# Optimization experiments

Hardware: AMD Instinct MI355X
Metric: run time of the kernel (lower is better)

The kernel has to match this reference:

```python
import jax, jax.numpy as jnp
import numpy as np

M_CENTER = 3.0  # diagonal value of the 'centers' matrix
OUT_HW = (513, 513)  # original input spatial size (input_shape in torch forward)


def _conv(x, w, dilation=1, padding=0):
    return jax.lax.conv_general_dilated(
        x, w, window_strides=(1, 1),
        padding=[(padding, padding), (padding, padding)],
        rhs_dilation=(dilation, dilation),
        dimension_numbers=("NCHW", "OIHW", "NCHW"))


def _resize(x, hw):
    return jax.image.resize(x, (x.shape[0], x.shape[1], hw[0], hw[1]), method="bilinear")


def _head(low_level, out, pw, w0, w1, w2, w3, pool_w, aproj_w, cw1, cw2, cb2):
    # DeepLabHeadV3Plus (BN folded to identity at inference: gamma=1, beta=0, mean=0, var=1)
    ll = jax.nn.relu(_conv(low_level, pw))                      # [N,48,129,129]
    branches = [jax.nn.relu(_conv(out, w0))]                    # 1x1 branch
    for w, d in zip((w1, w2, w3), (6, 12, 18)):
        branches.append(jax.nn.relu(_conv(out, w, dilation=d, padding=d)))
    gp = jnp.mean(out, axis=(2, 3), keepdims=True)              # AdaptiveAvgPool2d(1)
    gp = jax.nn.relu(_conv(gp, pool_w))
    gp = jnp.broadcast_to(gp, branches[0].shape)                # bilinear upsample of 1x1 == broadcast
    branches.append(gp)
    y = jax.nn.relu(_conv(jnp.concatenate(branches, axis=1), aproj_w))  # [N,256,33,33]
    y = _resize(y, (ll.shape[2], ll.shape[3]))                  # -> 129x129
    y = jnp.concatenate([ll, y], axis=1)                        # [N,304,129,129]
    y = jax.nn.relu(_conv(y, cw1, padding=1))
    y = _conv(y, cw2) + cb2[None, :, None, None]                # [N,C,129,129]
    return y


def _forward_single(x):
    # x: [N,C,129,129] head logits. Upsample, then squared-distance to diagonal centers (m*I).
    x = _resize(x, OUT_HW)                                      # [N,C,513,513]
    C = x.shape[1]
    features_out = jnp.transpose(x, (0, 2, 3, 1))               # NHWC, as in torch
    # dist2mean[...,c] = -sum_j (f_j - m*1[j==c])^2 = -(|f|^2 - 2*m*f_c + m^2)
    sumsq = jnp.sum(x * x, axis=1, keepdims=True)
    logits = 2.0 * M_CENTER * x - sumsq - M_CENTER * M_CENTER   # [N,C,513,513]
    centers = M_CENTER * jnp.eye(C, dtype=x.dtype)
    return logits, centers, features_out


def _kaiming(key, shape):
    fan_in = shape[1] * shape[2] * shape[3]
    return jax.random.normal(key, shape, jnp.float32) * np.sqrt(2.0 / fan_in)


def _head_params(key, num_classes):
    ks = jax.random.split(key, 10)
    return dict(
        pw=_kaiming(ks[0], (48, 256, 1, 1)),
        w0=_kaiming(ks[1], (256, 2048, 1, 1)),
        w1=_kaiming(ks[2], (256, 2048, 3, 3)),
        w2=_kaiming(ks[3], (256, 2048, 3, 3)),
        w3=_kaiming(ks[4], (256, 2048, 3, 3)),
        pool_w=_kaiming(ks[5], (256, 2048, 1, 1)),
        aproj_w=_kaiming(ks[6], (256, 1280, 1, 1)),
        cw1=_kaiming(ks[7], (256, 304, 3, 3)),
        cw2=_kaiming(ks[8], (num_classes, 256, 1, 1)),
        cb2=jnp.zeros((num_classes,), jnp.float32),
    )


def setup_inputs() -> dict:
    key = jax.random.key(0)
    k_ll, k_out, k_h0, k_h1 = jax.random.split(key, 4)
    inp = {
        "low_level": jax.random.normal(k_ll, (2, 256, 129, 129), jnp.float32),
        "out": jax.random.normal(k_out, (2, 2048, 33, 33), jnp.float32),
    }
    for pref, k, nc in (("h0_", k_h0, 16), ("h1_", k_h1, 17)):
        for name, v in _head_params(k, nc).items():
            inp[pref + name] = v
    return inp


def reference(low_level, out,
              h0_pw, h0_w0, h0_w1, h0_w2, h0_w3, h0_pool_w, h0_aproj_w, h0_cw1, h0_cw2, h0_cb2,
              h1_pw, h1_w0, h1_w1, h1_w2, h1_w3, h1_pool_w, h1_aproj_w, h1_cw1, h1_cw2, h1_cb2):
    x0 = _head(low_level, out, h0_pw, h0_w0, h0_w1, h0_w2, h0_w3, h0_pool_w, h0_aproj_w, h0_cw1, h0_cw2, h0_cb2)
    x1 = _head(low_level, out, h1_pw, h1_w0, h1_w1, h1_w2, h1_w3, h1_pool_w, h1_aproj_w, h1_cw1, h1_cw2, h1_cb2)
    l0, c0, f0 = _forward_single(x0)
    l1, c1, f1 = _forward_single(x1)
    return (l0, l1, c0, c1, f0, f1)
```

## Files before the change

### kernel.cpp

```cpp
#include <hip/hip_runtime.h>

#define TPB 256

typedef _Float16 f16;
typedef __attribute__((ext_vector_type(8))) _Float16 f16x8;
typedef __attribute__((ext_vector_type(16))) float f32x16;

#define GLD_LDS(g, l) __builtin_amdgcn_global_load_lds( \
    (const __attribute__((address_space(1))) void*)(g), \
    (__attribute__((address_space(3))) void*)(l), 16, 0, 0)

__global__ __launch_bounds__(TPB)
void tcz_k(const float* __restrict__ aspp, const float* __restrict__ ll,
           f16* __restrict__ Xa, f16* __restrict__ Xll, float* __restrict__ gp)
{
    const int bid = blockIdx.x;
    const int tid = threadIdx.x;
    __shared__ float t32[32 * 33];
    __shared__ float red[4];
    if (bid >= 12816) {
        const int bc = bid - 12816;
        const float* p = aspp + (size_t)bc * 1089;
        float s = 0.f;
        for (int i = tid; i < 1089; i += TPB) s += p[i];
#pragma unroll
        for (int off = 32; off > 0; off >>= 1) s += __shfl_down(s, off, 64);
        if ((tid & 63) == 0) red[tid >> 6] = s;
        __syncthreads();
        if (tid == 0) gp[bc] = (red[0] + red[1] + red[2] + red[3]) * (1.0f / 1089.0f);
        return;
    }
    const float* src; f16* dst; int C, HW, ldk, pT, cT, bb;
    if (bid < 4480) {
        src = aspp; dst = Xa; C = 2048; HW = 1089; ldk = 2048;
        pT = bid % 35; cT = (bid / 35) % 64; bb = bid / 2240;
    } else {
        const int b2 = bid - 4480;
        src = ll; dst = Xll; C = 256; HW = 16641; ldk = 256;
        pT = b2 % 521; cT = (b2 / 521) % 8; bb = b2 / 4168;
    }
#pragma unroll
    for (int pass = 0; pass < 4; ++pass) {
        const int ch = tid / 32 + pass * 8;
        const int px = tid % 32;
        const int c = cT * 32 + ch, p = pT * 32 + px;
        float v = 0.f;
        if (c < C && p < HW) v = src[((long)bb * C + c) * HW + p];
        t32[ch * 33 + px] = v;
    }
    __syncthreads();
#pragma unroll
    for (int pass = 0; pass < 4; ++pass) {
        const int px = tid / 32 + pass * 8;
        const int ch = tid % 32;
        const int p = pT * 32 + px, c = cT * 32 + ch;
        if (p < HW && c < C)
            dst[((long)bb * HW + p) * ldk + c] = (f16)t32[ch * 33 + px];
    }
}

__global__ __launch_bounds__(TPB)
void tcr_k(const f16* __restrict__ part, f16* __restrict__ dst)
{
    __shared__ float t32[32 * 33];
    const int pT = blockIdx.x, cT = blockIdx.y, bb = blockIdx.z;
    const int tid = threadIdx.x;
    const int br = cT >> 3;
    const f16* pb = part + (long)bb * 5575680;
#pragma unroll
    for (int pass = 0; pass < 4; ++pass) {
        const int ch = tid / 32 + pass * 8;
        const int px = tid % 32;
        const int c = cT * 32 + ch;
        const int cl = c & 255;
        const int p = pT * 32 + px;
        float v = 0.f;
        if (p < 1089) {
            const long cp = (long)cl * 1089 + p;
            if (br == 0) {
                v = (float)pb[cp] + (float)pb[278784 + cp];
            } else {
                const int dl = 6 * br;
                const int y = p / 33;
#pragma unroll
                for (int g = 0; g < 3; ++g) {
                    const int dy0 = (g - 1) * dl;
                    const int yLo = max(0, -dy0), yHi = min(33, 33 - dy0);
                    if (y >= yLo && y < yHi) {
                        const long s0 = (long)(2 * (1 + 3 * (br - 1) + g)) * 278784;
                        v += (float)pb[s0 + cp] + (float)pb[s0 + 278784 + cp];
                    }
                }
            }
            v = fmaxf(v, 0.f);
        }
        t32[ch * 33 + px] = v;
    }
    __syncthreads();
#pragma unroll
    for (int pass = 0; pass < 4; ++pass) {
        const int px = tid / 32 + pass * 8;
        const int ch = tid % 32;
        const int p = pT * 32 + px, c = cT * 32 + ch;
        if (p < 1089)
            dst[((long)bb * 1089 + p) * 1024 + c] = (f16)t32[ch * 33 + px];
    }
}

__global__ __launch_bounds__(TPB)
void gemv1_k(const float* __restrict__ pw0, const float* __restrict__ pw1,
             const float* __restrict__ gp, float* __restrict__ gpr2)
{
    const int bh = blockIdx.x & 3;
    const int cgrp = blockIdx.x >> 2;
    const int b = bh & 1;
    const float* w = (bh >> 1) ? pw1 : pw0;
    const int c = cgrp * 16 + (threadIdx.x >> 4);
    const int kl = threadIdx.x & 15;
    const float* g = gp + (size_t)b * 2048;
    float4 acc = {0.f, 0.f, 0.f, 0.f};
    for (int k = kl * 4; k < 2048; k += 64) {
        const float4 wv = *(const float4*)&w[(size_t)c * 2048 + k];
        const float4 gv = *(const float4*)&g[k];
        acc.x = fmaf(wv.x, gv.x, acc.x);
        acc.y = fmaf(wv.y, gv.y, acc.y);
        acc.z = fmaf(wv.z, gv.z, acc.z);
        acc.w = fmaf(wv.w, gv.w, acc.w);
    }
    float s = (acc.x + acc.y) + (acc.z + acc.w);
#pragma unroll
    for (int o = 8; o; o >>= 1) s += __shfl_xor(s, o, 16);
    if (kl == 0) gpr2[bh * 256 + c] = fmaxf(s, 0.f);
}

__global__ __launch_bounds__(TPB)
void gemv2_k(const float* __restrict__ ap0, const float* __restrict__ ap1,
             const float* __restrict__ gpr2, float* __restrict__ gpc2)
{
    const int bh = blockIdx.x & 3;
    const int cgrp = blockIdx.x >> 2;
    const float* w = (bh >> 1) ? ap1 : ap0;
    const int c = cgrp * 16 + (threadIdx.x >> 4);
    const int kl = threadIdx.x & 15;
    const float* g = gpr2 + bh * 256;
    float4 acc = {0.f, 0.f, 0.f, 0.f};
    for (int k = kl * 4; k < 256; k += 64) {
        const float4 wv = *(const float4*)&w[(size_t)c * 1280 + 1024 + k];
        const float4 gv = *(const float4*)&g[k];
        acc.x = fmaf(wv.x, gv.x, acc.x);
        acc.y = fmaf(wv.y, gv.y, acc.y);
        acc.z = fmaf(wv.z, gv.z, acc.z);
        acc.w = fmaf(wv.w, gv.w, acc.w);
    }
    float s = (acc.x + acc.y) + (acc.z + acc.w);
#pragma unroll
    for (int o = 8; o; o >>= 1) s += __shfl_xor(s, o, 16);
    if (kl == 0) gpc2[bh * 256 + c] = s;
}

struct PackJob { const float* w; f16* dst; int Cout, CinUse, CinSrc, T, coP, KB, start; };
struct PackParams { PackJob j[14]; };

__global__ __launch_bounds__(TPB)
void packw_mega(PackParams P, float* __restrict__ guard)
{
    const int bid = blockIdx.x;
    const int tid = threadIdx.x;
    if (bid >= 4832) {
        float4 zv = {0.f, 0.f, 0.f, 0.f};
        float4* p = (float4*)(guard + tid * 16);
        p[0] = zv; p[1] = zv; p[2] = zv; p[3] = zv;
        return;
    }
    int ji = 0;
#pragma unroll
    for (int t = 1; t < 14; ++t) if (bid >= P.j[t].start) ji = t;
    PackJob J;
    switch (ji) {
        case 0:  J = P.j[0];  break;
        case 1:  J = P.j[1];  break;
        case 2:  J = P.j[2];  break;
        case 3:  J = P.j[3];  break;
        case 4:  J = P.j[4];  break;
        case 5:  J = P.j[5];  break;
        case 6:  J = P.j[6];  break;
        case 7:  J = P.j[7];  break;
        case 8:  J = P.j[8];  break;
        case 9:  J = P.j[9];  break;
        case 10: J = P.j[10]; break;
        case 11: J = P.j[11]; break;
        case 12: J = P.j[12]; break;
        default: J = P.j[13]; break;
    }
    const int local = bid - J.start;
    const int kb = local % J.KB;
    const int coT = local / J.KB;
    const int T = J.T;
    __shared__ float tile[16 * 577];
    const int RL = 64 * T;
    const int n = 16 * RL;
    for (int idx = tid; idx < n; idx += TPB) {
        const int row = idx / RL;
        const int jj = idx - row * RL;
        const int co = coT * 16 + row;
        const int k = kb * 64 + jj / T;
        float v = 0.f;
        if (co < J.Cout && k < J.CinUse)
            v = J.w[((long)co * J.CinSrc + kb * 64) * T + jj];
        tile[row * 577 + jj] = v;
    }
    __syncthreads();
    const int nst = 128 * T;
    for (int idx = tid; idx < nst; idx += TPB) {
        const int g = idx & 7;
        const int t = (idx >> 3) % T;
        const int co = idx / (8 * T);
        f16x8 hv;
#pragma unroll
        for (int e = 0; e < 8; ++e)
            hv[e] = (f16)tile[co * 577 + (g * 8 + e) * T + t];
        *(f16x8*)&J.dst[(((long)t * J.KB + kb) * J.coP + coT * 16 + co) * 64 + g * 8] = hv;
    }
}

template <int OUTMODE, int ZMAP, int RELUOUT, int BIAS>
__global__ __launch_bounds__(TPB, 4)
void mconv(const f16* __restrict__ X, const f16* __restrict__ Wp,
           const f16* __restrict__ guard, void* __restrict__ out_,
           const float* __restrict__ gpc,
           int Cinp, int Cout, int H, int W, int kss_, int dl_,
           int kbPerTap, int tapCnt_,
           long xHstr, long wHstr, long oHstr, long outBStride,
           int coP, int ldOut, int NT, int NM, int NBH, int NZ)
{
    __shared__ char SH[32768];
    const int tid = threadIdx.x;

    int wg;
    {
        const int orig = blockIdx.x, nwg = gridDim.x;
        const int q = nwg >> 3, r = nwg & 7;
        const int xcd = orig & 7, off = orig >> 3;
        wg = (xcd < r ? xcd * (q + 1) : r * (q + 1) + (xcd - r) * q) + off;
    }
    const int nt = wg % NT; wg /= NT;
    const int mt = wg % NM; wg /= NM;
    const int bh = wg % NBH; wg /= NBH;
    const int z  = wg;
    const int b = bh & 1, hd = bh >> 1;
    const int co0 = mt * 128;
    const int NP = H * W;
    const long xBstr = (long)NP * Cinp;

    int kss = kss_, dl = dl_, tapStart = 0, tapCnt = tapCnt_;
    int kbB = 0, kbE = kbPerTap;
    long woff = (long)hd * wHstr, ooff = (long)hd * oHstr;
    int p0 = nt * 128, pMax = NP;
    if (ZMAP == 1) {
        const int zg = z >> 1, khf = z & 1;
        int br, grp;
        if (zg == 0) { br = 0; grp = 1; kss = 1; dl = 1; tapStart = 0; tapCnt = 1; }
        else { br = 1 + (zg - 1) / 3; grp = (zg - 1) % 3;
               kss = 3; dl = (br == 1) ? 6 : (br == 2 ? 12 : 18);
               tapStart = grp * 3; tapCnt = 3; }
        woff += (br == 0) ? 0L : (br == 1 ? 524288L : (br == 2 ? 5242880L : 9961472L));
        ooff += (long)z * 278784L;
        kbB = khf * (kbPerTap >> 1);
        kbE = kbB + (kbPerTap >> 1);
        const int dy0 = (kss == 1) ? 0 : (grp - 1) * dl;
        const int yLo = max(0, -dy0), yHi = min(H, H - dy0);
        p0 = yLo * W + nt * 128;
        pMax = yHi * W;
        if (p0 >= pMax) return;
    }
    const int half = kss >> 1;
    const int y0t = p0 / W, y1t = min(p0 + 127, pMax - 1) / W;

    int taps[9]; int nval = 0;
    for (int t = 0; t < tapCnt; ++t) {
        const int tp = tapStart + t;
        const int ky = tp / kss;
        const int dy = (ky - half) * dl;
        if (ZMAP == 1 || (y1t + dy >= 0 && y0t + dy < H)) taps[nval++] = tp;
    }
    if (nval == 0) return;

    const int srow = tid >> 3;
    const int sslot = tid & 7;
    int aofs[4];
#pragma unroll
    for (int q = 0; q < 4; ++q) {
        const int row = q * 32 + srow;
        aofs[q] = row * 64 + ((sslot ^ (row & 7)) << 3);
    }
    const long coStr = (long)coP * 64;

    const int lane = tid & 63, wid = tid >> 6;
    const int wm = wid >> 1, wn = wid & 1;
    const int r32 = lane & 31, hh = lane >> 5;
    const int arow0 = wm * 64 + r32, arow1 = arow0 + 32;
    const int brow0 = wn * 64 + r32, brow1 = brow0 + 32;
    const int abase0 = arow0 * 128, abase1 = arow1 * 128;
    const int bbase0 = 16384 + brow0 * 128, bbase1 = 16384 + brow1 * 128;
    const int ax0 = (arow0 & 7), ax1 = (arow1 & 7);
    const int bx0 = (brow0 & 7), bx1 = (brow1 & 7);

    f32x16 acc[2][2];
#pragma unroll
    for (int i = 0; i < 2; ++i)
#pragma unroll
        for (int j = 0; j < 2; ++j) acc[i][j] = (f32x16)(0.f);

    const f16* Pr[4];
    for (int ti = 0; ti < nval; ++ti) {
        const int tp = taps[ti];
        const int ky = tp / kss, kx = tp - ky * kss;
        const int dy = (ky - half) * dl, dx = (kx - half) * dl;
#pragma unroll
        for (int q = 0; q < 4; ++q) {
            const int row = q * 32 + srow;
            const int p = p0 + row;
            bool v = p < pMax;
            const int py = v ? p / W : 0;
            const int px = v ? p - py * W : 0;
            const int sy = py + dy, sx = px + dx;
            v = v && ((unsigned)sy < (unsigned)H) && ((unsigned)sx < (unsigned)W);
            const int swz = (sslot ^ (row & 7)) << 3;
            Pr[q] = v ? (X + (long)b * xBstr + (long)hd * xHstr
                           + ((long)sy * W + sx) * (long)Cinp + swz)
                      : (guard + swz);
        }
        const f16* Wt = Wp + woff + ((long)tp * kbPerTap * coP + (long)co0) * 64;
        for (int kb = kbB; kb < kbE; ++kb) {
            __syncthreads();
            const f16* wsrc = Wt + (long)kb * coStr;
            const long kcol = (long)kb << 6;
            GLD_LDS(wsrc + aofs[0], SH + (tid << 4));
            GLD_LDS(wsrc + aofs[1], SH + 4096 + (tid << 4));
            GLD_LDS(wsrc + aofs[2], SH + 8192 + (tid << 4));
            GLD_LDS(wsrc + aofs[3], SH + 12288 + (tid << 4));
            GLD_LDS(Pr[0] + kcol, SH + 16384 + (tid << 4));
            GLD_LDS(Pr[1] + kcol, SH + 20480 + (tid << 4));
            GLD_LDS(Pr[2] + kcol, SH + 24576 + (tid << 4));
            GLD_LDS(Pr[3] + kcol, SH + 28672 + (tid << 4));
            __syncthreads();
            __builtin_amdgcn_s_setprio(1);
#pragma unroll
            for (int kh = 0; kh < 4; ++kh) {
                const int g = kh * 2 + hh;
                const f16x8 a0 = *(const f16x8*)(SH + abase0 + ((g ^ ax0) << 4));
                const f16x8 a1 = *(const f16x8*)(SH + abase1 + ((g ^ ax1) << 4));
                const f16x8 b0 = *(const f16x8*)(SH + bbase0 + ((g ^ bx0) << 4));
                const f16x8 b1 = *(const f16x8*)(SH + bbase1 + ((g ^ bx1) << 4));
                acc[0][0] = __builtin_amdgcn_mfma_f32_32x32x16_f16(a0, b0, acc[0][0], 0, 0, 0);
                acc[0][1] = __builtin_amdgcn_mfma_f32_32x32x16_f16(a0, b1, acc[0][1], 0, 0, 0);
                acc[1][0] = __builtin_amdgcn_mfma_f32_32x32x16_f16(a1, b0, acc[1][0], 0, 0, 0);
                acc[1][1] = __builtin_amdgcn_mfma_f32_32x32x16_f16(a1, b1, acc[1][1], 0, 0, 0);
            }
            __builtin_amdgcn_s_setprio(0);
        }
    }

    const long outB = (long)b * outBStride + ooff;
    const float* gpcp = BIAS ? (gpc + (long)(b + 2 * hd) * 256) : nullptr;
#pragma unroll
    for (int mi = 0; mi < 2; ++mi)
#pragma unroll
    for (int ni = 0; ni < 2; ++ni)
#pragma unroll
    for (int j = 0; j < 16; ++j) {
        const int m = wm * 64 + mi * 32 + 4 * hh + (j & 3) + 8 * (j >> 2);
        const int n = wn * 64 + ni * 32 + r32;
        const int co = co0 + m;
        const int p = p0 + n;
        if (co < Cout && p < pMax) {
            float v = acc[mi][ni][j];
            if (BIAS) v += gpcp[co];
            if (RELUOUT) v = fmaxf(v, 0.f);
            if (OUTMODE == 1) ((f16*)out_)[outB + (long)co * NP + p] = (f16)v;
            else              ((f16*)out_)[outB + (long)p * ldOut + co] = (f16)v;
        }
    }
}

__global__ __launch_bounds__(TPB)
void ups2pad_k(const f16* __restrict__ ybx, f16* __restrict__ ccx)
{
    const int idx = blockIdx.x * TPB + threadIdx.x;
    if (idx >= 4 * 16641 * 34) return;
    const int s = idx / (16641 * 34);
    const int rem = idx - s * (16641 * 34);
    const int p = rem / 34;
    const int cg = rem - p * 34;
    if (cg >= 32) {
        f16x8 zv = (f16x8)(f16)0.f;
        *(f16x8*)(ccx + ((long)s * 16641 + p) * 320 + 304 + (cg - 32) * 8) = zv;
        return;
    }
    const int oy = p / 129, ox = p % 129;
    const float sc = 33.0f / 129.0f;
    const float sx = (ox + 0.5f) * sc - 0.5f;
    const float sy = (oy + 0.5f) * sc - 0.5f;
    int ix0 = (int)floorf(sx), iy0 = (int)floorf(sy);
    const float fx = sx - ix0, fy = sy - iy0;
    int ix1 = min(32, max(0, ix0 + 1)); ix0 = min(32, max(0, ix0));
    int iy1 = min(32, max(0, iy0 + 1)); iy0 = min(32, max(0, iy0));
    const f16* base = ybx + (long)s * 1089 * 256 + cg * 8;
    const f16x8 v00 = *(const f16x8*)(base + ((long)iy0 * 33 + ix0) * 256);
    const f16x8 v01 = *(const f16x8*)(base + ((long)iy0 * 33 + ix1) * 256);
    const f16x8 v10 = *(const f16x8*)(base + ((long)iy1 * 33 + ix0) * 256);
    const f16x8 v11 = *(const f16x8*)(base + ((long)iy1 * 33 + ix1) * 256);
    f16x8 r;
#pragma unroll
    for (int e = 0; e < 8; ++e) {
        const float a0 = (float)v00[e] + ((float)v01[e] - (float)v00[e]) * fx;
        const float a1 = (float)v10[e] + ((float)v11[e] - (float)v10[e]) * fx;
        r[e] = (f16)(a0 + (a1 - a0) * fy);
    }
    *(f16x8*)(ccx + ((long)s * 16641 + p) * 320 + 48 + cg * 8) = r;
}

__global__ __launch_bounds__(TPB)
void conv1x1_m(const f16* __restrict__ c1o2,
               const float* __restrict__ w0, const float* __restrict__ w1,
               const float* __restrict__ b0, const float* __restrict__ b1,
               float* __restrict__ xb2)
{
    const int h = blockIdx.z;
    const int nc = h ? 17 : 16;
    const float* w = h ? w1 : w0;
    const float* bias = h ? b1 : b0;
    __shared__ float wsm[256 * 17];
    __shared__ float bsm[17];
    const int tid = threadIdx.x;
    for (int l = tid; l < 256 * 17; l += TPB) {
        const int k = l / 17, c = l - k * 17;
        wsm[l] = (c < nc) ? w[(size_t)c * 256 + k] : 0.f;
    }
    if (tid < nc) bsm[tid] = bias[tid];
    __syncthreads();
    const int b = blockIdx.y;
    const int p = blockIdx.x * TPB + tid;
    if (p >= 16641) return;
    const f16* inB = c1o2 + (long)h * 8520192 + (long)b * 4260096 + p;
    float acc[17];
#pragma unroll
    for (int c = 0; c < 17; ++c) acc[c] = 0.f;
    for (int k = 0; k < 256; ++k) {
        const float x = (float)inB[(size_t)k * 16641];
#pragma unroll
        for (int c = 0; c < 17; ++c) acc[c] = fmaf(wsm[k * 17 + c], x, acc[c]);
    }
    float* oB = xb2 + (h ? 532512L : 0L) + ((long)b * nc) * 16641 + p;
#pragma unroll
    for (int c = 0; c < 17; ++c)
        if (c < nc) oB[(size_t)c * 16641] = acc[c] + bsm[c];
}

__global__ __launch_bounds__(TPB)
void final_m(const float* __restrict__ xb2, float* __restrict__ o)
{
    const int idx = blockIdx.x * TPB + threadIdx.x;
    if (idx >= 2 * 526338) return;
    const int hd = idx / 526338;
    int r = idx - hd * 526338;
    const int ox = r % 513; r /= 513;
    const int oy = r % 513;
    const int b = r / 513;
    const int nc = hd ? 17 : 16;
    const long HW = 513L * 513L;
    const float sc = 129.0f / 513.0f;
    const float sx = (ox + 0.5f) * sc - 0.5f;
    const float sy = (oy + 0.5f) * sc - 0.5f;
    int ix0 = (int)floorf(sx), iy0 = (int)floorf(sy);
    const float fx = sx - ix0, fy = sy - iy0;
    int ix1 = min(128, max(0, ix0 + 1)); ix0 = min(128, max(0, ix0));
    int iy1 = min(128, max(0, iy0 + 1)); iy0 = min(128, max(0, iy0));
    const float* xb = xb2 + (hd ? 532512L : 0L) + (size_t)b * nc * 16641;
    const int i00 = iy0 * 129 + ix0, i01 = iy0 * 129 + ix1;
    const int i10 = iy1 * 129 + ix0, i11 = iy1 * 129 + ix1;
    float* logits = o + (hd ? 8421408L : 0L);
    float* feats  = o + (hd ? 25791107L : 17369699L);
    float v[17];
    float ss = 0.f;
#pragma unroll
    for (int c = 0; c < 17; ++c) {
        if (c < nc) {
            const float* s = xb + (size_t)c * 16641;
            const float a0 = s[i00] + (s[i01] - s[i00]) * fx;
            const float a1 = s[i10] + (s[i11] - s[i10]) * fx;
            const float vv = a0 + (a1 - a0) * fy;
            v[c] = vv;
            ss = fmaf(vv, vv, ss);
        }
    }
    const long pix = (long)oy * 513 + ox;
#pragma unroll
    for (int c = 0; c < 17; ++c)
        if (c < nc)
            logits[((size_t)b * nc + c) * HW + pix] = fmaf(6.f, v[c], -ss - 9.f);
    float* f = feats + ((size_t)b * HW + pix) * nc;
#pragma unroll
    for (int c = 0; c < 17; ++c)
        if (c < nc) f[c] = v[c];
}

__global__ void centers_k(float* __restrict__ c0, float* __restrict__ c1)
{
    const int t = blockIdx.x * 64 + threadIdx.x;
    if (t < 256) c0[t] = (t / 16 == t % 16) ? 3.f : 0.f;
    const int u = t - 256;
    if (u >= 0 && u < 289) c1[u] = (u / 17 == u % 17) ? 3.f : 0.f;
}

extern "C" void kernel_launch(void* const* d_in, const int* in_sizes, int n_in,
                              void* d_out, int out_size, void* d_ws, size_t ws_size,
                              hipStream_t stream)
{
    const float* low_level = (const float*)d_in[0];
    const float* aspp_in   = (const float*)d_in[1];
    float* ws = (float*)d_ws;
    float* o  = (float*)d_out;

    float* GUARDF  = ws + 0;
    f16*   GUARD   = (f16*)GUARDF;
    f16*   Apack2  = (f16*)(ws + 4096);
    f16*   C1O2    = (f16*)(ws + 4096);
    f16*   AprojP2 = (f16*)(ws + 14684160);
    f16*   Cw1P2   = (f16*)(ws + 14946304);
    f16*   LlP2    = (f16*)(ws + 15683584);
    f16*   Xa      = (f16*)(ws + 15716352);
    f16*   BRX2    = (f16*)(ws + 17946624);
    f16*   YBX2    = (f16*)(ws + 20176896);
    float* XB2     = ws + 20734464;
    float* GP      = ws + 21832770;
    float* GPC2    = ws + 21836866;
    float* GPR2    = ws + 21837890;

    f16*   CCX2    = (f16*)(o + 0);
    f16*   Xll     = (f16*)(o + 10650240);
    f16*   BRpart  = (f16*)(o + 14910336);

    const long C0o = 17369154, C1oo = 17369410;

    tcz_k<<<16912, TPB, 0, stream>>>(aspp_in, low_level, Xa, Xll, GP);
    gemv1_k<<<64, TPB, 0, stream>>>(
        (const float*)d_in[2 + 5], (const float*)d_in[2 + 10 + 5], GP, GPR2);
    gemv2_k<<<64, TPB, 0, stream>>>(
        (const float*)d_in[2 + 6], (const float*)d_in[2 + 10 + 6], GPR2, GPC2);

    PackParams P;
    int start = 0;
    for (int h = 0; h < 2; ++h) {
        const float* pw    = (const float*)d_in[2 + h * 10 + 0];
        const float* w0    = (const float*)d_in[2 + h * 10 + 1];
        const float* w1    = (const float*)d_in[2 + h * 10 + 2];
        const float* w2    = (const float*)d_in[2 + h * 10 + 3];
        const float* w3    = (const float*)d_in[2 + h * 10 + 4];
        const float* aproj = (const float*)d_in[2 + h * 10 + 6];
        const float* cw1   = (const float*)d_in[2 + h * 10 + 7];
        f16* Ap = Apack2 + (long)h * 14680064;
        const PackJob jobs[7] = {
            { w0,    Ap,                          256, 2048, 2048, 1, 256, 32, 0 },
            { w1,    Ap + 524288,                 256, 2048, 2048, 9, 256, 32, 0 },
            { w2,    Ap + 5242880,                256, 2048, 2048, 9, 256, 32, 0 },
            { w3,    Ap + 9961472,                256, 2048, 2048, 9, 256, 32, 0 },
            { aproj, AprojP2 + (long)h * 262144,  256, 1024, 1280, 1, 256, 16, 0 },
            { cw1,   Cw1P2 + (long)h * 737280,    256,  304,  304, 9, 256,  5, 0 },
            { pw,    LlP2 + (long)h * 32768,       48,  256,  256, 1, 128,  4, 0 },
        };
        for (int t = 0; t < 7; ++t) {
            P.j[h * 7 + t] = jobs[t];
            P.j[h * 7 + t].start = start;
            start += jobs[t].KB * (jobs[t].coP / 16);
        }
    }
    packw_mega<<<4833, TPB, 0, stream>>>(P, GUARDF);

    mconv<1, 1, 0, 0><<<1440, TPB, 0, stream>>>(
        Xa, Apack2, GUARD, BRpart, nullptr, 2048, 256, 33, 33, 3, 1,
        32, 0, 0L, 14680064L, 11151360L, 5575680L, 256, 0, 9, 2, 4, 20);
    tcr_k<<<dim3(35, 32, 4), TPB, 0, stream>>>(BRpart, BRX2);
    mconv<3, 0, 1, 1><<<72, TPB, 0, stream>>>(
        BRX2, AprojP2, GUARD, YBX2, GPC2, 1024, 256, 33, 33, 1, 1,
        16, 1, 2230272L, 262144L, 557568L, 278784L, 256, 256, 9, 2, 4, 1);
    mconv<3, 0, 1, 0><<<524, TPB, 0, stream>>>(
        Xll, LlP2, GUARD, CCX2, nullptr, 256, 48, 129, 129, 1, 1,
        4, 1, 0L, 32768L, 10650240L, 5325120L, 128, 320, 131, 1, 4, 1);
    ups2pad_k<<<8841, TPB, 0, stream>>>(YBX2, CCX2);
    mconv<1, 0, 1, 0><<<1048, TPB, 0, stream>>>(
        CCX2, Cw1P2, GUARD, C1O2, nullptr, 320, 256, 129, 129, 3, 1,
        5, 9, 10650240L, 737280L, 8520192L, 4260096L, 256, 0, 131, 2, 4, 1);
    conv1x1_m<<<dim3(66, 2, 2), TPB, 0, stream>>>(C1O2,
        (const float*)d_in[2 + 8], (const float*)d_in[2 + 10 + 8],
        (const float*)d_in[2 + 9], (const float*)d_in[2 + 10 + 9], XB2);
    final_m<<<4113, TPB, 0, stream>>>(XB2, o);
    centers_k<<<9, 64, 0, stream>>>(o + C0o, o + C1oo);
}
```

Measured before the change: 633.8 us.

## Split aproj GEMM over K, vectorize weight pack, shrink conv1x1 blocks

The ASPP projection GEMM is split into two K halves via a new ZMAP=2 mode, doubling its grid from 72 to 144 blocks. The partial outputs are summed with ReLU inside the bilinear upsample kernel, and bias is added only in the first half. The weight-pack kernel now loads float4 rows for jobs other than the 304-channel one, with the LDS tile stride padded to 580. conv1x1_m now runs 128-thread blocks with twice as many blocks. Together these target underutilised small launches, at the cost of an extra partial buffer and doubled loads in the upsample kernel.

Result: faster. 578.5 us (-8.7%).

```diff
diff --git a/kernel.cpp b/kernel.cpp
--- a/kernel.cpp
+++ b/kernel.cpp
@@ -196,18 +196,32 @@
     const int kb = local % J.KB;
     const int coT = local / J.KB;
     const int T = J.T;
-    __shared__ float tile[16 * 577];
+    __shared__ float tile[16 * 580];
     const int RL = 64 * T;
-    const int n = 16 * RL;
-    for (int idx = tid; idx < n; idx += TPB) {
-        const int row = idx / RL;
-        const int jj = idx - row * RL;
-        const int co = coT * 16 + row;
-        const int k = kb * 64 + jj / T;
-        float v = 0.f;
-        if (co < J.Cout && k < J.CinUse)
-            v = J.w[((long)co * J.CinSrc + kb * 64) * T + jj];
-        tile[row * 577 + jj] = v;
+    if (J.CinUse != 304) {
+        const int RL4 = RL >> 2;
+        const int n4 = 16 * RL4;
+        for (int idx = tid; idx < n4; idx += TPB) {
+            const int row = idx / RL4;
+            const int j4 = idx - row * RL4;
+            const int co = coT * 16 + row;
+            float4 v = {0.f, 0.f, 0.f, 0.f};
+            if (co < J.Cout)
+                v = *(const float4*)&J.w[((long)co * J.CinSrc + kb * 64) * T + j4 * 4];
+            *(float4*)&tile[row * 580 + j4 * 4] = v;
+        }
+    } else {
+        const int n = 16 * RL;
+        for (int idx = tid; idx < n; idx += TPB) {
+            const int row = idx / RL;
+            const int jj = idx - row * RL;
+            const int co = coT * 16 + row;
+            const int k = kb * 64 + jj / T;
+            float v = 0.f;
+            if (co < J.Cout && k < J.CinUse)
+                v = J.w[((long)co * J.CinSrc + kb * 64) * T + jj];
+            tile[row * 580 + jj] = v;
+        }
     }
     __syncthreads();
     const int nst = 128 * T;
@@ -218,7 +232,7 @@
         f16x8 hv;
 #pragma unroll
         for (int e = 0; e < 8; ++e)
-            hv[e] = (f16)tile[co * 577 + (g * 8 + e) * T + t];
+            hv[e] = (f16)tile[co * 580 + (g * 8 + e) * T + t];
         *(f16x8*)&J.dst[(((long)t * J.KB + kb) * J.coP + coT * 16 + co) * 64 + g * 8] = hv;
     }
 }
@@ -230,7 +244,7 @@
            const float* __restrict__ gpc,
            int Cinp, int Cout, int H, int W, int kss_, int dl_,
            int kbPerTap, int tapCnt_,
-           long xHstr, long wHstr, long oHstr, long outBStride,
+           long xHstr, long wHstr, long oHstr, long outBStride, long zStr,
            int coP, int ldOut, int NT, int NM, int NBH, int NZ)
 {
     __shared__ char SH[32768];
@@ -272,6 +286,10 @@
         p0 = yLo * W + nt * 128;
         pMax = yHi * W;
         if (p0 >= pMax) return;
+    } else if (ZMAP == 2) {
+        kbB = z * (kbPerTap >> 1);
+        kbE = kbB + (kbPerTap >> 1);
+        ooff += (long)z * zStr;
     }
     const int half = kss >> 1;
     const int y0t = p0 / W, y1t = min(p0 + 127, pMax - 1) / W;
@@ -375,7 +393,7 @@
         const int p = p0 + n;
         if (co < Cout && p < pMax) {
             float v = acc[mi][ni][j];
-            if (BIAS) v += gpcp[co];
+            if (BIAS && (ZMAP != 2 || z == 0)) v += gpcp[co];
             if (RELUOUT) v = fmaxf(v, 0.f);
             if (OUTMODE == 1) ((f16*)out_)[outB + (long)co * NP + p] = (f16)v;
             else              ((f16*)out_)[outB + (long)p * ldOut + co] = (f16)v;
@@ -405,22 +423,31 @@
     const float fx = sx - ix0, fy = sy - iy0;
     int ix1 = min(32, max(0, ix0 + 1)); ix0 = min(32, max(0, ix0));
     int iy1 = min(32, max(0, iy0 + 1)); iy0 = min(32, max(0, iy0));
-    const f16* base = ybx + (long)s * 1089 * 256 + cg * 8;
-    const f16x8 v00 = *(const f16x8*)(base + ((long)iy0 * 33 + ix0) * 256);
-    const f16x8 v01 = *(const f16x8*)(base + ((long)iy0 * 33 + ix1) * 256);
-    const f16x8 v10 = *(const f16x8*)(base + ((long)iy1 * 33 + ix0) * 256);
-    const f16x8 v11 = *(const f16x8*)(base + ((long)iy1 * 33 + ix1) * 256);
+    const f16* base = ybx + (long)s * 278784 + cg * 8;
+    const f16* base2 = base + 1115136;
+    const long i00 = ((long)iy0 * 33 + ix0) * 256;
+    const long i01 = ((long)iy0 * 33 + ix1) * 256;
+    const long i10 = ((long)iy1 * 33 + ix0) * 256;
+    const long i11 = ((long)iy1 * 33 + ix1) * 256;
+    const f16x8 a00 = *(const f16x8*)(base + i00), b00 = *(const f16x8*)(base2 + i00);
+    const f16x8 a01 = *(const f16x8*)(base + i01), b01 = *(const f16x8*)(base2 + i01);
+    const f16x8 a10 = *(const f16x8*)(base + i10), b10 = *(const f16x8*)(base2 + i10);
+    const f16x8 a11 = *(const f16x8*)(base + i11), b11 = *(const f16x8*)(base2 + i11);
     f16x8 r;
 #pragma unroll
     for (int e = 0; e < 8; ++e) {
-        const float a0 = (float)v00[e] + ((float)v01[e] - (float)v00[e]) * fx;
-        const float a1 = (float)v10[e] + ((float)v11[e] - (float)v10[e]) * fx;
-        r[e] = (f16)(a0 + (a1 - a0) * fy);
+        const float v00 = fmaxf((float)a00[e] + (float)b00[e], 0.f);
+        const float v01 = fmaxf((float)a01[e] + (float)b01[e], 0.f);
+        const float v10 = fmaxf((float)a10[e] + (float)b10[e], 0.f);
+        const float v11 = fmaxf((float)a11[e] + (float)b11[e], 0.f);
+        const float q0 = v00 + (v01 - v00) * fx;
+        const float q1 = v10 + (v11 - v10) * fx;
+        r[e] = (f16)(q0 + (q1 - q0) * fy);
     }
     *(f16x8*)(ccx + ((long)s * 16641 + p) * 320 + 48 + cg * 8) = r;
 }
 
-__global__ __launch_bounds__(TPB)
+__global__ __launch_bounds__(128)
 void conv1x1_m(const f16* __restrict__ c1o2,
                const float* __restrict__ w0, const float* __restrict__ w1,
                const float* __restrict__ b0, const float* __restrict__ b1,
@@ -433,14 +460,14 @@
     __shared__ float wsm[256 * 17];
     __shared__ float bsm[17];
     const int tid = threadIdx.x;
-    for (int l = tid; l < 256 * 17; l += TPB) {
+    for (int l = tid; l < 256 * 17; l += 128) {
         const int k = l / 17, c = l - k * 17;
         wsm[l] = (c < nc) ? w[(size_t)c * 256 + k] : 0.f;
     }
     if (tid < nc) bsm[tid] = bias[tid];
     __syncthreads();
     const int b = blockIdx.y;
-    const int p = blockIdx.x * TPB + tid;
+    const int p = blockIdx.x * 128 + tid;
     if (p >= 16641) return;
     const f16* inB = c1o2 + (long)h * 8520192 + (long)b * 4260096 + p;
     float acc[17];
@@ -532,10 +559,10 @@
     f16*   Xa      = (f16*)(ws + 15716352);
     f16*   BRX2    = (f16*)(ws + 17946624);
     f16*   YBX2    = (f16*)(ws + 20176896);
-    float* XB2     = ws + 20734464;
-    float* GP      = ws + 21832770;
-    float* GPC2    = ws + 21836866;
-    float* GPR2    = ws + 21837890;
+    float* XB2     = ws + 21292032;
+    float* GP      = ws + 22390338;
+    float* GPC2    = ws + 22394434;
+    float* GPR2    = ws + 22395458;
 
     f16*   CCX2    = (f16*)(o + 0);
     f16*   Xll     = (f16*)(o + 10650240);
@@ -579,19 +606,19 @@
 
     mconv<1, 1, 0, 0><<<1440, TPB, 0, stream>>>(
         Xa, Apack2, GUARD, BRpart, nullptr, 2048, 256, 33, 33, 3, 1,
-        32, 0, 0L, 14680064L, 11151360L, 5575680L, 256, 0, 9, 2, 4, 20);
+        32, 0, 0L, 14680064L, 11151360L, 5575680L, 0L, 256, 0, 9, 2, 4, 20);
     tcr_k<<<dim3(35, 32, 4), TPB, 0, stream>>>(BRpart, BRX2);
-    mconv<3, 0, 1, 1><<<72, TPB, 0, stream>>>(
+    mconv<3, 2, 0, 1><<<144, TPB, 0, stream>>>(
         BRX2, AprojP2, GUARD, YBX2, GPC2, 1024, 256, 33, 33, 1, 1,
-        16, 1, 2230272L, 262144L, 557568L, 278784L, 256, 256, 9, 2, 4, 1);
+        16, 1, 2230272L, 262144L, 557568L, 278784L, 1115136L, 256, 256, 9, 2, 4, 2);
     mconv<3, 0, 1, 0><<<524, TPB, 0, stream>>>(
         Xll, LlP2, GUARD, CCX2, nullptr, 256, 48, 129, 129, 1, 1,
-        4, 1, 0L, 32768L, 10650240L, 5325120L, 128, 320, 131, 1, 4, 1);
+        4, 1, 0L, 32768L, 10650240L, 5325120L, 0L, 128, 320, 131, 1, 4, 1);
     ups2pad_k<<<8841, TPB, 0, stream>>>(YBX2, CCX2);
     mconv<1, 0, 1, 0><<<1048, TPB, 0, stream>>>(
         CCX2, Cw1P2, GUARD, C1O2, nullptr, 320, 256, 129, 129, 3, 1,
-        5, 9, 10650240L, 737280L, 8520192L, 4260096L, 256, 0, 131, 2, 4, 1);
-    conv1x1_m<<<dim3(66, 2, 2), TPB, 0, stream>>>(C1O2,
+        5, 9, 10650240L, 737280L, 8520192L, 4260096L, 0L, 256, 0, 131, 2, 4, 1);
+    conv1x1_m<<<dim3(131, 2, 2), 128, 0, stream>>>(C1O2,
         (const float*)d_in[2 + 8], (const float*)d_in[2 + 10 + 8],
         (const float*)d_in[2 + 9], (const float*)d_in[2 + 10 + 9], XB2);
     final_m<<<4113, TPB, 0, stream>>>(XB2, o);
```
